# Kernel tuning notes

Measured on AMD Instinct MI355X. Metric: run time of the kernel, lower is better.

The kernel has to match this reference:

```python
import jax, jax.numpy as jnp
import numpy as np

N_NODES = 100000
N_EDGES = 1600000
IN_DIM = 128
OUT_DIM = 128


def setup_inputs() -> dict:
    key = jax.random.key(0)
    k1, k2, k3, k4 = jax.random.split(key, 4)
    # xavier-uniform-like init scales
    lim_W = float(np.sqrt(6.0 / (IN_DIM + OUT_DIM)))
    lim_a = float(np.sqrt(6.0 / (2 * OUT_DIM + 1)))
    inputs = {
        "input": jax.random.normal(k1, (N_NODES, IN_DIM), dtype=jnp.float32),
        "W": jax.random.uniform(k2, (IN_DIM, OUT_DIM), dtype=jnp.float32, minval=-lim_W, maxval=lim_W),
        "a": jax.random.uniform(k3, (2 * OUT_DIM, 1), dtype=jnp.float32, minval=-lim_a, maxval=lim_a),
        "triple": jax.random.randint(k4, (N_EDGES, 3), 0, N_NODES, dtype=jnp.int64 if jax.config.read('jax_enable_x64') else jnp.int32),
    }
    return inputs


def reference(input, W, a, triple):
    N = input.shape[0]
    d = W.shape[1]
    h = triple[:, 0]  # edge source (softmax segment / row of sparse matrix)
    t = triple[:, 2]  # edge destination (gathered neighbor)

    x = input @ W  # [N, d] projected features

    # e = leaky_relu(cat([x[h], x[t]]) @ a) computed without materializing [E, 2d]:
    s_src = (x @ a[:d]).squeeze(-1)  # [N]
    s_dst = (x @ a[d:]).squeeze(-1)  # [N]
    e = jax.nn.leaky_relu(s_src[h] + s_dst[t], negative_slope=0.2)  # [E]

    # sparse softmax over rows (segments = head node h)
    m = jax.ops.segment_max(e, h, num_segments=N)          # [N]
    ex = jnp.exp(e - m[h])                                  # [E]
    denom = jax.ops.segment_sum(ex, h, num_segments=N)     # [N]
    att = ex / denom[h]                                     # [E]

    # scatter-aggregate weighted neighbor features
    agg = jax.ops.segment_sum(att[:, None] * x[t], h, num_segments=N)  # [N, d]

    return jax.nn.elu(agg + x)
```

## Files before the change

kernel.cpp:

```cpp
#include <hip/hip_runtime.h>
#include <hip/hip_bf16.h>
#include <math.h>

#define IN_DIM 128
#define OUT_DIM 128
#define BM 64

#define BSHIFT 9
#define BNODES 512
#define CAP 12288
#define EPT 16
#define PPT 24

typedef short bf16x8s __attribute__((ext_vector_type(8)));
typedef float f32x4 __attribute__((ext_vector_type(4)));
typedef unsigned short u16;
typedef unsigned char u8;

__device__ inline unsigned int rne_hi(float f) {
    unsigned int u = __float_as_uint(f);
    return u + 0x7fffu + ((u >> 16) & 1u);
}
__device__ inline unsigned int pack_bf16x2(float lo, float hi) {
    return (rne_hi(lo) >> 16) | (rne_hi(hi) & 0xffff0000u);
}
__device__ inline float byf(unsigned int u, int sh) {
    return (float)((u >> sh) & 0xffu);
}

__global__ void wt_kernel(const float* __restrict__ W, u16* __restrict__ Wt)
{
    int k = blockIdx.x;
    int c = threadIdx.x;
    Wt[c * IN_DIM + k] = (u16)(rne_hi(W[k * OUT_DIM + c]) >> 16);
}

__global__ __launch_bounds__(256) void gemm_scatter_kernel(
    const float* __restrict__ in, const u16* __restrict__ WtG,
    const float* __restrict__ a, u8* __restrict__ xq, float* __restrict__ ssx,
    float* __restrict__ ssrc, float* __restrict__ sdst,
    const int* __restrict__ triple, int* __restrict__ coarse_cur,
    uint2* __restrict__ pairs, int N, int E, int nbc, int nScat)
{
    const int tid = threadIdx.x;

    if ((int)blockIdx.x < nScat) {
        __shared__ int cnt[256];
        __shared__ int base[256];
        const int cbase = blockIdx.x * (256 * EPT);

        cnt[tid] = 0;
        __syncthreads();

        int h[EPT], t[EPT], pos[EPT];
#pragma unroll
        for (int it = 0; it < EPT; ++it) {
            int idx = cbase + it * 256 + tid;
            if (idx < E) {
                h[it] = triple[3 * idx];
                t[it] = triple[3 * idx + 2];
                pos[it] = atomicAdd(&cnt[h[it] >> BSHIFT], 1);
            }
        }
        __syncthreads();
        if (tid < nbc && cnt[tid] > 0)
            base[tid] = tid * CAP + atomicAdd(&coarse_cur[tid], cnt[tid]);
        __syncthreads();
#pragma unroll
        for (int it = 0; it < EPT; ++it) {
            int idx = cbase + it * 256 + tid;
            if (idx < E)
                pairs[base[h[it] >> BSHIFT] + pos[it]] =
                    make_uint2((unsigned)h[it], (unsigned)t[it]);
        }
        return;
    }

    __shared__ u16 Al[BM][IN_DIM + 8];
    __shared__ u16 Wl[OUT_DIM][IN_DIM + 8];

    const int gb   = blockIdx.x - nScat;
    const int lane = tid & 63;
    const int wave = tid >> 6;
    const int rl   = lane & 15;
    const int rgrp = lane >> 4;

    {
        int r = tid >> 1, c0 = (tid & 1) * 64;
        const uint4* src = (const uint4*)(WtG + r * IN_DIM + c0);
        uint4* dst = (uint4*)&Wl[r][c0];
#pragma unroll
        for (int u = 0; u < 8; u++) dst[u] = src[u];
    }
    const long long rowbase = (long long)gb * BM;
    {
#pragma unroll
        for (int u = 0; u < 8; u++) {
            int idx = u * 256 + tid;
            int r = idx >> 5;
            int c = (idx & 31) * 4;
            long long gr = rowbase + r;
            if (gr >= N) gr = N - 1;
            float4 v = *(const float4*)(in + gr * IN_DIM + c);
            *(uint2*)&Al[r][c] = make_uint2(pack_bf16x2(v.x, v.y), pack_bf16x2(v.z, v.w));
        }
    }
    __syncthreads();

    f32x4 acc[8] = {};
#pragma unroll
    for (int ks = 0; ks < 4; ks++) {
        bf16x8s af = *(const bf16x8s*)&Al[wave * 16 + rl][ks * 32 + rgrp * 8];
#pragma unroll
        for (int cb = 0; cb < 8; cb++) {
            bf16x8s bf = *(const bf16x8s*)&Wl[cb * 16 + rl][ks * 32 + rgrp * 8];
            acc[cb] = __builtin_amdgcn_mfma_f32_16x16x32_bf16(af, bf, acc[cb], 0, 0, 0);
        }
    }

    float a_sv[8], a_dv[8];
#pragma unroll
    for (int cb = 0; cb < 8; cb++) {
        a_sv[cb] = a[rl + 16 * cb];
        a_dv[cb] = a[OUT_DIM + rl + 16 * cb];
    }
#pragma unroll
    for (int r = 0; r < 4; r++) {
        long long grow = rowbase + wave * 16 + rgrp * 4 + r;
        float ps = 0.f, pd = 0.f, rm = 0.f;
#pragma unroll
        for (int cb = 0; cb < 8; cb++) {
            float v = acc[cb][r];
            ps += v * a_sv[cb];
            pd += v * a_dv[cb];
            rm = fmaxf(rm, fabsf(v));
        }
#pragma unroll
        for (int off = 1; off < 16; off <<= 1) {
            ps += __shfl_xor(ps, off);
            pd += __shfl_xor(pd, off);
            rm = fmaxf(rm, __shfl_xor(rm, off));
        }
        rm = fmaxf(rm, 1e-20f);
        const float inv = 127.0f / rm;
        if (grow < N) {
#pragma unroll
            for (int cb = 0; cb < 8; cb++)
                xq[grow * OUT_DIM + rl + 16 * cb] =
                    (u8)(int)(fmaf(acc[cb][r], inv, 128.5f));
            if (rl == 0) {
                ssrc[grow] = ps;
                sdst[grow] = pd;
                ssx[grow]  = rm * (1.0f / 127.0f);
            }
        }
    }
}

__global__ __launch_bounds__(512) void bucket_csr_kernel(
    const uint2* __restrict__ pairs, const int* __restrict__ coarse_cur,
    int* __restrict__ startp, int* __restrict__ edge_t, int N, int E, int nbc)
{
    __shared__ int cnt[BNODES];
    __shared__ int scn[BNODES];
    __shared__ int cursor[BNODES];
    __shared__ int bsum[256];
    const int b = blockIdx.x;
    const int tid = threadIdx.x;
    const int plo = b * CAP;
    const int psz = coarse_cur[b];

    uint2 myp[PPT];
#pragma unroll
    for (int jj = 0; jj < PPT; ++jj) {
        int idx = jj * BNODES + tid;
        if (idx < psz) myp[jj] = pairs[plo + idx];
    }

    if (tid < 256) bsum[tid] = (tid < nbc) ? coarse_cur[tid] : 0;
    __syncthreads();
#pragma unroll
    for (int off = 1; off < 256; off <<= 1) {
        int v = 0;
        if (tid < 256 && tid >= off) v = bsum[tid - off];
        __syncthreads();
        if (tid < 256 && tid >= off) bsum[tid] += v;
        __syncthreads();
    }
    const int obase = bsum[b] - psz;

    cnt[tid] = 0;
    __syncthreads();
#pragma unroll
    for (int jj = 0; jj < PPT; ++jj) {
        int idx = jj * BNODES + tid;
        if (idx < psz) atomicAdd(&cnt[myp[jj].x & (BNODES - 1)], 1);
    }
    __syncthreads();
    scn[tid] = cnt[tid];
    __syncthreads();
#pragma unroll
    for (int off = 1; off < BNODES; off <<= 1) {
        int v = (tid >= off) ? scn[tid - off] : 0;
        __syncthreads();
        scn[tid] += v;
        __syncthreads();
    }
    const int excl = scn[tid] - cnt[tid];
    const int node = b * BNODES + tid;
    if (node < N) startp[node] = obase + excl;
    cursor[tid] = obase + excl;
    __syncthreads();
#pragma unroll
    for (int jj = 0; jj < PPT; ++jj) {
        int idx = jj * BNODES + tid;
        if (idx < psz) {
            int pos = atomicAdd(&cursor[myp[jj].x & (BNODES - 1)], 1);
            edge_t[pos] = (int)myp[jj].y;
        }
    }
    if (b == 0 && tid == 0) startp[N] = E;
}

__global__ __launch_bounds__(256) void aggregate_kernel(
    const u8* __restrict__ xq, const float* __restrict__ ssx,
    const float* __restrict__ ssrc, const float* __restrict__ sdst,
    const int* __restrict__ startp, const int* __restrict__ edge_t,
    float* __restrict__ out, int N)
{
    const int wid  = threadIdx.x >> 6;
    const int lane = threadIdx.x & 63;
    const int i0 = (blockIdx.x * 4 + wid) * 2;
    if (i0 >= N) return;
    const int half = lane >> 5;
    const int l32  = lane & 31;
    const int iH   = i0 + half;
    const bool hasH = iH < N;
    const int j16 = lane & 15;

    int lo = 0, hi = 0;
    if (hasH) { lo = startp[iH]; hi = startp[iH + 1]; }
    const int deg = hi - lo;
    const int degO = __shfl_xor(deg, 32);
    const int degMax = __builtin_amdgcn_readfirstlane(max(deg, degO));

    float acc[8];
#pragma unroll
    for (int d = 0; d < 8; d++) acc[d] = 0.f;

    if (degMax <= 32) {
        const float si = hasH ? ssrc[iH] : 0.f;
        bool act = l32 < deg;
        int t = act ? edge_t[lo + l32] : 0;
        float sde = act ? sdst[t] : 0.f;
        float ssl = act ? ssx[t] : 0.f;
        float e = act ? si + sde : -INFINITY;
        e = (e > 0.f) ? e : 0.2f * e;
        float m = e;
#pragma unroll
        for (int off = 16; off; off >>= 1) m = fmaxf(m, __shfl_xor(m, off));
        float p = act ? __expf(e - m) : 0.f;
        float den = p;
#pragma unroll
        for (int off = 16; off; off >>= 1) den += __shfl_xor(den, off);
        float w = (deg > 0) ? p / den : 0.f;
        float cs = w * ssl;
        float Ss = cs;
#pragma unroll
        for (int off = 16; off; off >>= 1) Ss += __shfl_xor(Ss, off);

        const int slot = (lane >> 4) & 1;
        const int srcBase = half << 5;
        const u8* xj = xq + j16 * 8;
        const int nb = (degMax + 1) >> 1;

        uint2 v[16];
        float cc[16];
#pragma unroll
        for (int bb = 0; bb < 16; ++bb) {
            if (bb < nb) {
                int ei = bb * 2 + slot;
                int tt = __shfl(t, srcBase + ei);
                cc[bb] = __shfl(cs, srcBase + ei);
                v[bb] = *(const uint2*)(xj + (size_t)tt * OUT_DIM);
            }
        }
#pragma unroll
        for (int bb = 0; bb < 16; ++bb) {
            if (bb < nb) {
                float c = cc[bb];
                acc[0] += c * byf(v[bb].x, 0);
                acc[1] += c * byf(v[bb].x, 8);
                acc[2] += c * byf(v[bb].x, 16);
                acc[3] += c * byf(v[bb].x, 24);
                acc[4] += c * byf(v[bb].y, 0);
                acc[5] += c * byf(v[bb].y, 8);
                acc[6] += c * byf(v[bb].y, 16);
                acc[7] += c * byf(v[bb].y, 24);
            }
        }

#pragma unroll
        for (int d = 0; d < 8; d++) acc[d] += __shfl_xor(acc[d], 16);

        if (!(lane & 16) && hasH) {
            float ssi = ssx[iH];
            float r0 = -128.f * Ss - 128.f * ssi;
            uint2 rv = *(const uint2*)(xq + (size_t)iH * OUT_DIM + j16 * 8);
            float o[8];
            o[0] = fmaf(ssi, byf(rv.x, 0),  acc[0] + r0);
            o[1] = fmaf(ssi, byf(rv.x, 8),  acc[1] + r0);
            o[2] = fmaf(ssi, byf(rv.x, 16), acc[2] + r0);
            o[3] = fmaf(ssi, byf(rv.x, 24), acc[3] + r0);
            o[4] = fmaf(ssi, byf(rv.y, 0),  acc[4] + r0);
            o[5] = fmaf(ssi, byf(rv.y, 8),  acc[5] + r0);
            o[6] = fmaf(ssi, byf(rv.y, 16), acc[6] + r0);
            o[7] = fmaf(ssi, byf(rv.y, 24), acc[7] + r0);
#pragma unroll
            for (int d = 0; d < 8; d++)
                o[d] = (o[d] > 0.f) ? o[d] : __expf(o[d]) - 1.f;
            float* dst = out + (size_t)iH * OUT_DIM + j16 * 8;
            *(float4*)(dst)     = make_float4(o[0], o[1], o[2], o[3]);
            *(float4*)(dst + 4) = make_float4(o[4], o[5], o[6], o[7]);
        }
        return;
    }

    const int eg = lane >> 4;
    for (int h = 0; h < 2; ++h) {
        const int i = i0 + h;
        if (i >= N) break;
        const int slo = startp[i];
        const int shi = startp[i + 1];
        const int sdeg = shi - slo;
        const float si = ssrc[i];
        float S128 = 0.f;

#pragma unroll
        for (int d = 0; d < 8; d++) acc[d] = 0.f;
        const u8* xj = xq + j16 * 8;

        if (sdeg > 0 && sdeg <= 64) {
            int j = slo + lane;
            bool act = j < shi;
            int t = act ? edge_t[j] : 0;
            float ssl = act ? ssx[t] : 0.f;
            float e = act ? si + sdst[t] : -INFINITY;
            e = (e > 0.f) ? e : 0.2f * e;
            float m = e;
#pragma unroll
            for (int off = 32; off; off >>= 1) m = fmaxf(m, __shfl_xor(m, off));
            float p = act ? __expf(e - m) : 0.f;
            float den = p;
#pragma unroll
            for (int off = 32; off; off >>= 1) den += __shfl_xor(den, off);
            float cs = (p / den) * ssl;
            float Ss = cs;
#pragma unroll
            for (int off = 32; off; off >>= 1) Ss += __shfl_xor(Ss, off);
            S128 = 128.f * Ss;

            int nit = (sdeg + 3) >> 2;
            for (int it = 0; it < nit; ++it) {
                int ei = it * 4 + eg;
                int tt = __shfl(t, ei);
                float c = __shfl(cs, ei);
                if (ei < sdeg) {
                    uint2 v = *(const uint2*)(xj + (size_t)tt * OUT_DIM);
                    acc[0] += c * byf(v.x, 0);
                    acc[1] += c * byf(v.x, 8);
                    acc[2] += c * byf(v.x, 16);
                    acc[3] += c * byf(v.x, 24);
                    acc[4] += c * byf(v.y, 0);
                    acc[5] += c * byf(v.y, 8);
                    acc[6] += c * byf(v.y, 16);
                    acc[7] += c * byf(v.y, 24);
                }
            }
        } else if (sdeg > 64) {
            float m = -INFINITY;
            for (int j = slo + lane; j < shi; j += 64) {
                int t = edge_t[j];
                float e = si + sdst[t];
                e = (e > 0.f) ? e : 0.2f * e;
                m = fmaxf(m, e);
            }
#pragma unroll
            for (int off = 32; off; off >>= 1) m = fmaxf(m, __shfl_xor(m, off));
            float den = 0.f, sS = 0.f;
            for (int j = slo + lane; j < shi; j += 64) {
                int t = edge_t[j];
                float e = si + sdst[t];
                e = (e > 0.f) ? e : 0.2f * e;
                float p = __expf(e - m);
                den += p;
                sS = fmaf(p, ssx[t], sS);
            }
#pragma unroll
            for (int off = 32; off; off >>= 1) {
                den += __shfl_xor(den, off);
                sS  += __shfl_xor(sS, off);
            }
            const float invden = 1.f / den;
            S128 = 128.f * sS * invden;

            for (int jj = slo; jj < shi; jj += 4) {
                int ei = jj + eg;
                if (ei < shi) {
                    int tt = edge_t[ei];
                    float e = si + sdst[tt];
                    e = (e > 0.f) ? e : 0.2f * e;
                    float c = __expf(e - m) * invden * ssx[tt];
                    uint2 v = *(const uint2*)(xj + (size_t)tt * OUT_DIM);
                    acc[0] += c * byf(v.x, 0);
                    acc[1] += c * byf(v.x, 8);
                    acc[2] += c * byf(v.x, 16);
                    acc[3] += c * byf(v.x, 24);
                    acc[4] += c * byf(v.y, 0);
                    acc[5] += c * byf(v.y, 8);
                    acc[6] += c * byf(v.y, 16);
                    acc[7] += c * byf(v.y, 24);
                }
            }
        }

#pragma unroll
        for (int d = 0; d < 8; d++) acc[d] += __shfl_xor(acc[d], 16);
#pragma unroll
        for (int d = 0; d < 8; d++) acc[d] += __shfl_xor(acc[d], 32);

        if (lane < 16) {
            float ssi = ssx[i];
            float r0 = -S128 - 128.f * ssi;
            uint2 rv = *(const uint2*)(xq + (size_t)i * OUT_DIM + j16 * 8);
            float o[8];
            o[0] = fmaf(ssi, byf(rv.x, 0),  acc[0] + r0);
            o[1] = fmaf(ssi, byf(rv.x, 8),  acc[1] + r0);
            o[2] = fmaf(ssi, byf(rv.x, 16), acc[2] + r0);
            o[3] = fmaf(ssi, byf(rv.x, 24), acc[3] + r0);
            o[4] = fmaf(ssi, byf(rv.y, 0),  acc[4] + r0);
            o[5] = fmaf(ssi, byf(rv.y, 8),  acc[5] + r0);
            o[6] = fmaf(ssi, byf(rv.y, 16), acc[6] + r0);
            o[7] = fmaf(ssi, byf(rv.y, 24), acc[7] + r0);
#pragma unroll
            for (int d = 0; d < 8; d++)
                o[d] = (o[d] > 0.f) ? o[d] : __expf(o[d]) - 1.f;
            float* dst = out + (size_t)i * OUT_DIM + j16 * 8;
            *(float4*)(dst)     = make_float4(o[0], o[1], o[2], o[3]);
            *(float4*)(dst + 4) = make_float4(o[4], o[5], o[6], o[7]);
        }
    }
}

extern "C" void kernel_launch(void* const* d_in, const int* in_sizes, int n_in,
                              void* d_out, int out_size, void* d_ws, size_t ws_size,
                              hipStream_t stream)
{
    const float* input  = (const float*)d_in[0];
    const float* W      = (const float*)d_in[1];
    const float* a      = (const float*)d_in[2];
    const int*   triple = (const int*)d_in[3];
    const int N = in_sizes[0] / IN_DIM;
    const int E = in_sizes[3] / 3;
    float* out = (float*)d_out;

    const int NBC = (N + BNODES - 1) >> BSHIFT;

    char* p = (char*)d_ws;
    auto carve = [&](size_t bytes) {
        char* q = p;
        p += (bytes + 15) & ~(size_t)15;
        return q;
    };
    u8*   xq        = (u8*)carve((size_t)N * OUT_DIM);
    u16*  Wt        = (u16*)carve((size_t)IN_DIM * OUT_DIM * sizeof(u16));
    float* ssx      = (float*)carve((size_t)N * sizeof(float));
    float* ssrc     = (float*)carve((size_t)N * sizeof(float));
    float* sdst     = (float*)carve((size_t)N * sizeof(float));
    int*  startp    = (int*)carve((size_t)(N + 1) * sizeof(int));
    int*  coarse_cur= (int*)carve(256 * sizeof(int));
    int*  edge_t    = (int*)carve((size_t)E * sizeof(int));
    uint2* pairs    = (uint2*)carve((size_t)NBC * CAP * sizeof(uint2));

    const int nScat = (E + 256 * EPT - 1) / (256 * EPT);
    const int nGemm = (N + BM - 1) / BM;

    hipMemsetAsync(coarse_cur, 0, 256 * sizeof(int), stream);
    wt_kernel<<<IN_DIM, OUT_DIM, 0, stream>>>(W, Wt);
    gemm_scatter_kernel<<<nScat + nGemm, 256, 0, stream>>>(
        input, Wt, a, xq, ssx, ssrc, sdst, triple, coarse_cur, pairs, N, E, NBC, nScat);
    bucket_csr_kernel<<<NBC, BNODES, 0, stream>>>(pairs, coarse_cur, startp, edge_t, N, E, NBC);
    aggregate_kernel<<<(N + 7) / 8, 256, 0, stream>>>(xq, ssx, ssrc, sdst, startp, edge_t, out, N);
}
```

Measured before the change: 115.7 us.

## Pack edge pairs to 32-bit, interleave per-node scalars, use wave-level scans

Each bucketed edge pair is packed into one 32-bit word (local head index in the high bits, tail in the low 17 bits), halving the pairs buffer traffic. The sdst and ssx arrays are merged into one float2 array, so every gathered neighbor needs a single 8-byte load instead of two scattered loads. The block-wide shared-memory scans in the bucket kernel are replaced with shuffle-based wave scans, cutting syncthreads. The memset is folded into wt_kernel to drop one launch. The 17-bit tail field assumes N is at most 131072.

```diff
diff --git a/kernel.cpp b/kernel.cpp
--- a/kernel.cpp
+++ b/kernel.cpp
@@ -16,6 +16,7 @@
 typedef float f32x4 __attribute__((ext_vector_type(4)));
 typedef unsigned short u16;
 typedef unsigned char u8;
+typedef unsigned int u32;
 
 __device__ inline unsigned int rne_hi(float f) {
     unsigned int u = __float_as_uint(f);
@@ -28,19 +29,22 @@
     return (float)((u >> sh) & 0xffu);
 }
 
-__global__ void wt_kernel(const float* __restrict__ W, u16* __restrict__ Wt)
+__global__ void wt_kernel(const float* __restrict__ W, u16* __restrict__ Wt,
+                          int* __restrict__ coarse_cur)
 {
     int k = blockIdx.x;
     int c = threadIdx.x;
-    Wt[c * IN_DIM + k] = (u16)(rne_hi(W[k * OUT_DIM + c]) >> 16);
+    int ii = k * OUT_DIM + c;
+    if (ii < 256) coarse_cur[ii] = 0;
+    Wt[c * IN_DIM + k] = (u16)(rne_hi(W[ii]) >> 16);
 }
 
 __global__ __launch_bounds__(256) void gemm_scatter_kernel(
     const float* __restrict__ in, const u16* __restrict__ WtG,
-    const float* __restrict__ a, u8* __restrict__ xq, float* __restrict__ ssx,
-    float* __restrict__ ssrc, float* __restrict__ sdst,
+    const float* __restrict__ a, u8* __restrict__ xq,
+    float* __restrict__ ssrc, float2* __restrict__ sds,
     const int* __restrict__ triple, int* __restrict__ coarse_cur,
-    uint2* __restrict__ pairs, int N, int E, int nbc, int nScat)
+    u32* __restrict__ pairs, int N, int E, int nbc, int nScat)
 {
     const int tid = threadIdx.x;
 
@@ -71,7 +75,7 @@
             int idx = cbase + it * 256 + tid;
             if (idx < E)
                 pairs[base[h[it] >> BSHIFT] + pos[it]] =
-                    make_uint2((unsigned)h[it], (unsigned)t[it]);
+                    ((u32)(h[it] & (BNODES - 1)) << 17) | (u32)t[it];
         }
         return;
     }
@@ -150,83 +154,96 @@
                     (u8)(int)(fmaf(acc[cb][r], inv, 128.5f));
             if (rl == 0) {
                 ssrc[grow] = ps;
-                sdst[grow] = pd;
-                ssx[grow]  = rm * (1.0f / 127.0f);
+                sds[grow]  = make_float2(pd, rm * (1.0f / 127.0f));
             }
         }
     }
 }
 
 __global__ __launch_bounds__(512) void bucket_csr_kernel(
-    const uint2* __restrict__ pairs, const int* __restrict__ coarse_cur,
+    const u32* __restrict__ pairs, const int* __restrict__ coarse_cur,
     int* __restrict__ startp, int* __restrict__ edge_t, int N, int E, int nbc)
 {
     __shared__ int cnt[BNODES];
-    __shared__ int scn[BNODES];
     __shared__ int cursor[BNODES];
-    __shared__ int bsum[256];
+    __shared__ int wsum[8];
+    __shared__ int obase_s;
     const int b = blockIdx.x;
     const int tid = threadIdx.x;
+    const int wv  = tid >> 6;
+    const int ln  = tid & 63;
     const int plo = b * CAP;
     const int psz = coarse_cur[b];
 
-    uint2 myp[PPT];
+    u32 myp[PPT];
 #pragma unroll
     for (int jj = 0; jj < PPT; ++jj) {
         int idx = jj * BNODES + tid;
         if (idx < psz) myp[jj] = pairs[plo + idx];
     }
 
-    if (tid < 256) bsum[tid] = (tid < nbc) ? coarse_cur[tid] : 0;
-    __syncthreads();
-#pragma unroll
-    for (int off = 1; off < 256; off <<= 1) {
-        int v = 0;
-        if (tid < 256 && tid >= off) v = bsum[tid - off];
+    {
+        int v = (tid < b) ? coarse_cur[tid] : 0;
+#pragma unroll
+        for (int off = 32; off; off >>= 1) v += __shfl_xor(v, off);
+        if (ln == 0) wsum[wv] = v;
         __syncthreads();
-        if (tid < 256 && tid >= off) bsum[tid] += v;
-        __syncthreads();
-    }
-    const int obase = bsum[b] - psz;
+        if (tid == 0) {
+            int s = 0;
+#pragma unroll
+            for (int w = 0; w < 8; w++) s += wsum[w];
+            obase_s = s;
+        }
+    }
 
     cnt[tid] = 0;
     __syncthreads();
 #pragma unroll
     for (int jj = 0; jj < PPT; ++jj) {
         int idx = jj * BNODES + tid;
-        if (idx < psz) atomicAdd(&cnt[myp[jj].x & (BNODES - 1)], 1);
+        if (idx < psz) atomicAdd(&cnt[myp[jj] >> 17], 1);
     }
     __syncthreads();
-    scn[tid] = cnt[tid];
+
+    const int myCnt = cnt[tid];
+    int sc = myCnt;
+#pragma unroll
+    for (int off = 1; off < 64; off <<= 1) {
+        int u = __shfl_up(sc, off);
+        if (ln >= off) sc += u;
+    }
+    if (ln == 63) wsum[wv] = sc;
     __syncthreads();
-#pragma unroll
-    for (int off = 1; off < BNODES; off <<= 1) {
-        int v = (tid >= off) ? scn[tid - off] : 0;
-        __syncthreads();
-        scn[tid] += v;
-        __syncthreads();
-    }
-    const int excl = scn[tid] - cnt[tid];
+    int wbase = 0;
+    {
+#pragma unroll
+        for (int w = 0; w < 8; w++) {
+            int s = wsum[w];
+            if (w < wv) wbase += s;
+        }
+    }
+    const int obase = obase_s;
+    const int excl = obase + wbase + sc - myCnt;
     const int node = b * BNODES + tid;
-    if (node < N) startp[node] = obase + excl;
-    cursor[tid] = obase + excl;
+    if (node < N) startp[node] = excl;
+    cursor[tid] = excl;
     __syncthreads();
 #pragma unroll
     for (int jj = 0; jj < PPT; ++jj) {
         int idx = jj * BNODES + tid;
         if (idx < psz) {
-            int pos = atomicAdd(&cursor[myp[jj].x & (BNODES - 1)], 1);
-            edge_t[pos] = (int)myp[jj].y;
+            u32 p = myp[jj];
+            int pos = atomicAdd(&cursor[p >> 17], 1);
+            edge_t[pos] = (int)(p & 0x1FFFFu);
         }
     }
     if (b == 0 && tid == 0) startp[N] = E;
 }
 
 __global__ __launch_bounds__(256) void aggregate_kernel(
-    const u8* __restrict__ xq, const float* __restrict__ ssx,
-    const float* __restrict__ ssrc, const float* __restrict__ sdst,
-    const int* __restrict__ startp, const int* __restrict__ edge_t,
-    float* __restrict__ out, int N)
+    const u8* __restrict__ xq, const float* __restrict__ ssrc,
+    const float2* __restrict__ sds, const int* __restrict__ startp,
+    const int* __restrict__ edge_t, float* __restrict__ out, int N)
 {
     const int wid  = threadIdx.x >> 6;
     const int lane = threadIdx.x & 63;
@@ -252,9 +269,8 @@
         const float si = hasH ? ssrc[iH] : 0.f;
         bool act = l32 < deg;
         int t = act ? edge_t[lo + l32] : 0;
-        float sde = act ? sdst[t] : 0.f;
-        float ssl = act ? ssx[t] : 0.f;
-        float e = act ? si + sde : -INFINITY;
+        float2 sv = act ? sds[t] : make_float2(0.f, 0.f);
+        float e = act ? si + sv.x : -INFINITY;
         e = (e > 0.f) ? e : 0.2f * e;
         float m = e;
 #pragma unroll
@@ -264,7 +280,7 @@
 #pragma unroll
         for (int off = 16; off; off >>= 1) den += __shfl_xor(den, off);
         float w = (deg > 0) ? p / den : 0.f;
-        float cs = w * ssl;
+        float cs = w * sv.y;
         float Ss = cs;
 #pragma unroll
         for (int off = 16; off; off >>= 1) Ss += __shfl_xor(Ss, off);
@@ -304,7 +320,7 @@
         for (int d = 0; d < 8; d++) acc[d] += __shfl_xor(acc[d], 16);
 
         if (!(lane & 16) && hasH) {
-            float ssi = ssx[iH];
+            float ssi = sds[iH].y;
             float r0 = -128.f * Ss - 128.f * ssi;
             uint2 rv = *(const uint2*)(xq + (size_t)iH * OUT_DIM + j16 * 8);
             float o[8];
@@ -344,8 +360,8 @@
             int j = slo + lane;
             bool act = j < shi;
             int t = act ? edge_t[j] : 0;
-            float ssl = act ? ssx[t] : 0.f;
-            float e = act ? si + sdst[t] : -INFINITY;
+            float2 sv = act ? sds[t] : make_float2(0.f, 0.f);
+            float e = act ? si + sv.x : -INFINITY;
             e = (e > 0.f) ? e : 0.2f * e;
             float m = e;
 #pragma unroll
@@ -354,7 +370,7 @@
             float den = p;
 #pragma unroll
             for (int off = 32; off; off >>= 1) den += __shfl_xor(den, off);
-            float cs = (p / den) * ssl;
+            float cs = (p / den) * sv.y;
             float Ss = cs;
 #pragma unroll
             for (int off = 32; off; off >>= 1) Ss += __shfl_xor(Ss, off);
@@ -381,7 +397,7 @@
             float m = -INFINITY;
             for (int j = slo + lane; j < shi; j += 64) {
                 int t = edge_t[j];
-                float e = si + sdst[t];
+                float e = si + sds[t].x;
                 e = (e > 0.f) ? e : 0.2f * e;
                 m = fmaxf(m, e);
             }
@@ -390,11 +406,12 @@
             float den = 0.f, sS = 0.f;
             for (int j = slo + lane; j < shi; j += 64) {
                 int t = edge_t[j];
-                float e = si + sdst[t];
+                float2 sv = sds[t];
+                float e = si + sv.x;
                 e = (e > 0.f) ? e : 0.2f * e;
                 float p = __expf(e - m);
                 den += p;
-                sS = fmaf(p, ssx[t], sS);
+                sS = fmaf(p, sv.y, sS);
             }
 #pragma unroll
             for (int off = 32; off; off >>= 1) {
@@ -408,9 +425,10 @@
                 int ei = jj + eg;
                 if (ei < shi) {
                     int tt = edge_t[ei];
-                    float e = si + sdst[tt];
+                    float2 sv = sds[tt];
+                    float e = si + sv.x;
                     e = (e > 0.f) ? e : 0.2f * e;
-                    float c = __expf(e - m) * invden * ssx[tt];
+                    float c = __expf(e - m) * invden * sv.y;
                     uint2 v = *(const uint2*)(xj + (size_t)tt * OUT_DIM);
                     acc[0] += c * byf(v.x, 0);
                     acc[1] += c * byf(v.x, 8);
@@ -430,7 +448,7 @@
         for (int d = 0; d < 8; d++) acc[d] += __shfl_xor(acc[d], 32);
 
         if (lane < 16) {
-            float ssi = ssx[i];
+            float ssi = sds[i].y;
             float r0 = -S128 - 128.f * ssi;
             uint2 rv = *(const uint2*)(xq + (size_t)i * OUT_DIM + j16 * 8);
             float o[8];
@@ -472,23 +490,21 @@
         p += (bytes + 15) & ~(size_t)15;
         return q;
     };
-    u8*   xq        = (u8*)carve((size_t)N * OUT_DIM);
-    u16*  Wt        = (u16*)carve((size_t)IN_DIM * OUT_DIM * sizeof(u16));
-    float* ssx      = (float*)carve((size_t)N * sizeof(float));
-    float* ssrc     = (float*)carve((size_t)N * sizeof(float));
-    float* sdst     = (float*)carve((size_t)N * sizeof(float));
-    int*  startp    = (int*)carve((size_t)(N + 1) * sizeof(int));
-    int*  coarse_cur= (int*)carve(256 * sizeof(int));
-    int*  edge_t    = (int*)carve((size_t)E * sizeof(int));
-    uint2* pairs    = (uint2*)carve((size_t)NBC * CAP * sizeof(uint2));
+    u8*    xq        = (u8*)carve((size_t)N * OUT_DIM);
+    u16*   Wt        = (u16*)carve((size_t)IN_DIM * OUT_DIM * sizeof(u16));
+    float* ssrc      = (float*)carve((size_t)N * sizeof(float));
+    float2* sds      = (float2*)carve((size_t)N * sizeof(float2));
+    int*   startp    = (int*)carve((size_t)(N + 1) * sizeof(int));
+    int*   coarse_cur= (int*)carve(256 * sizeof(int));
+    int*   edge_t    = (int*)carve((size_t)E * sizeof(int));
+    u32*   pairs     = (u32*)carve((size_t)NBC * CAP * sizeof(u32));
 
     const int nScat = (E + 256 * EPT - 1) / (256 * EPT);
     const int nGemm = (N + BM - 1) / BM;
 
-    hipMemsetAsync(coarse_cur, 0, 256 * sizeof(int), stream);
-    wt_kernel<<<IN_DIM, OUT_DIM, 0, stream>>>(W, Wt);
+    wt_kernel<<<IN_DIM, OUT_DIM, 0, stream>>>(W, Wt, coarse_cur);
     gemm_scatter_kernel<<<nScat + nGemm, 256, 0, stream>>>(
-        input, Wt, a, xq, ssx, ssrc, sdst, triple, coarse_cur, pairs, N, E, NBC, nScat);
+        input, Wt, a, xq, ssrc, sds, triple, coarse_cur, pairs, N, E, NBC, nScat);
     bucket_csr_kernel<<<NBC, BNODES, 0, stream>>>(pairs, coarse_cur, startp, edge_t, N, E, NBC);
-    aggregate_kernel<<<(N + 7) / 8, 256, 0, stream>>>(xq, ssx, ssrc, sdst, startp, edge_t, out, N);
-}
+    aggregate_kernel<<<(N + 7) / 8, 256, 0, stream>>>(xq, ssrc, sds, startp, edge_t, out, N);
+}
```

After: 107.7 us. 6.9% less time.
